# Optimization experiments

Hardware: AMD Instinct MI355X
Metric: run time of the kernel (lower is better)

Reference implementation:

```python
import jax, jax.numpy as jnp
import numpy as np

X_CH, Y_CH = 3, 31
C = X_CH + Y_CH            # s_channels = m_channels = 34
A = C * (C - 1) // 2       # 561 Givens rotation angles
SMIN, SMAX = 0.001, 1000.0


def setup_inputs() -> dict:
    key = jax.random.key(0)
    k1, k2 = jax.random.split(key)
    x = jax.random.normal(k1, (4, X_CH, 64, 64), dtype=jnp.float32)
    W = jax.random.normal(k2, (C + C + A, X_CH), dtype=jnp.float32) * 0.1
    b = jnp.zeros((C + C + A,), dtype=jnp.float32)
    return {"x": x, "W": W, "b": b}


def _covariance(s, a):
    # s: (B, C, H, W) positive variances; a: (B, A, H, W) rotation angles.
    B, _, H, Wd = s.shape
    cs = jnp.moveaxis(jnp.cos(a), 1, 0)  # (A, B, H, W)
    ss = jnp.moveaxis(jnp.sin(a), 1, 0)  # (A, B, H, W)
    ii, jj = np.triu_indices(C, k=1)      # same (i, j) order as the torch double loop
    ii = jnp.asarray(ii, dtype=jnp.int32)
    jj = jnp.asarray(jj, dtype=jnp.int32)

    # R starts as identity; each Givens rotation rij only mixes columns i and j
    # of R (R <- R @ rij), so we update two columns instead of a full matmul.
    R0 = jnp.broadcast_to(jnp.eye(C, dtype=s.dtype), (B, H, Wd, C, C))

    def step(R, inp):
        c_, s_, i, j = inp
        col_i = R[..., i]                      # (B, H, W, C)
        col_j = R[..., j]
        c_ = c_[..., None]
        s_ = s_[..., None]
        R = R.at[..., i].set(c_ * col_i + s_ * col_j)
        R = R.at[..., j].set(-s_ * col_i + c_ * col_j)
        return R, None

    R, _ = jax.lax.scan(step, R0, (cs, ss, ii, jj))
    sp = jnp.transpose(s, (0, 2, 3, 1))        # (B, H, W, C)
    # S = R^T D R with D = diag(sp): S[k,n] = sum_m R[m,k] * sp[m] * R[m,n]
    S = jnp.einsum('bhwmk,bhwm,bhwmn->bhwkn', R, sp, R)
    D = jnp.zeros((B, H, Wd, C, C), dtype=s.dtype).at[..., jnp.arange(C), jnp.arange(C)].set(sp)
    return S, R, D


def reference(x, W, b):
    # 1x1-conv encoder: (B, 3, H, W) -> (B, 629, H, W)
    w = jnp.einsum('oc,bchw->bohw', W, x) + b[None, :, None, None]
    m = jnp.transpose(w[:, :C], (0, 2, 3, 1))                  # (B, H, W, C) mean
    s = jax.nn.sigmoid(w[:, C:2 * C])
    s = SMIN * (1.0 - s) + SMAX * s                            # (B, C, H, W)
    a = jnp.pi * jnp.tanh(w[:, 2 * C:])                        # (B, A, H, W)
    S, _, _ = _covariance(s, a)
    return m, S, s
```

## Files before the change

kernel.cpp:

```cpp
#include <hip/hip_runtime.h>


#define CCH 34
#define ACH 561
#define HWPIX 4096
#define NPIX 16384
#define PXB 14
#define NPR 7
#define NTHR 256
#define CSLEN 141
#define CSPAIR (CSLEN * 16)
#define VROW 36
#define VPX (17 * VROW * 4)
#define OFF_S 557056
#define OFF_s 19496960
#define LOG2E 1.4426950408889634f

typedef float    f32x2 __attribute__((ext_vector_type(2)));
typedef _Float16 h2    __attribute__((ext_vector_type(2)));

struct Pairs {
    short i[ACH]; short j[ACH];
    constexpr Pairs() : i(), j() {
        int p = 0;
        for (int a = 0; a < CCH - 1; ++a)
            for (int b = a + 1; b < CCH; ++b) { i[p] = (short)a; j[p] = (short)b; ++p; }
    }
};
__device__ constexpr Pairs PR{};

__device__ __forceinline__ float dot2h(h2 a, h2 b, float c) {
#if __has_builtin(__builtin_amdgcn_fdot2)
    return __builtin_amdgcn_fdot2(a, b, c, false);
#else
    return fmaf((float)a[0], (float)b[0], fmaf((float)a[1], (float)b[1], c));
#endif
}

__device__ __forceinline__ void rot2(f32x2& Ri, f32x2& Rj, f32x2 c2, f32x2 s2) {
    f32x2 t1, t2;
    asm("v_pk_mul_f32 %0, %1, %2" : "=v"(t1) : "v"(s2), "v"(Rj));
    asm("v_pk_mul_f32 %0, %1, %2" : "=v"(t2) : "v"(s2), "v"(Ri));
    asm("v_pk_fma_f32 %0, %1, %2, %3" : "=v"(Ri) : "v"(c2), "v"(Ri), "v"(t1));
    asm("v_pk_fma_f32 %0, %1, %2, %3 neg_lo:[0,0,1] neg_hi:[0,0,1]"
        : "=v"(Rj) : "v"(c2), "v"(Rj), "v"(t2));
}

template <int P0, int P1>
__device__ __forceinline__ void apply_rots(f32x2* R2, const float4* cs) {
    #pragma unroll
    for (int k = P0; k < P1; ++k) {
        float4 cc = cs[k - P0];
        f32x2 c2; c2[0] = cc.x; c2[1] = cc.y;
        f32x2 s2; s2[0] = cc.z; s2[1] = cc.w;
        rot2(R2[PR.i[k]], R2[PR.j[k]], c2, s2);
    }
}

__device__ __forceinline__ float2 cs_of(float wv) {
    float e  = __builtin_amdgcn_exp2f((2.0f * LOG2E) * wv);
    float tt = 1.0f - 2.0f * __builtin_amdgcn_rcpf(e + 1.0f);
    float rv = 0.5f * tt;
    return make_float2(__builtin_amdgcn_cosf(rv), __builtin_amdgcn_sinf(rv));
}

template <int G0, int LEN>
__device__ __forceinline__ void fill_cs(const float* __restrict__ Wm,
                                        const float* __restrict__ bvec,
                                        const float* xs, char* ldsbuf,
                                        int npr, int t) {
    for (int o = t; o < npr * LEN; o += NTHR) {
        int pr = (int)((unsigned)o / (unsigned)LEN);
        int l  = o - pr * LEN;
        int ch = 2 * CCH + G0 + l;
        float w0 = Wm[ch * 3 + 0], w1 = Wm[ch * 3 + 1], w2 = Wm[ch * 3 + 2];
        float bb = bvec[ch];
        int pa = 2 * pr, pb = 2 * pr + 1;
        float2 A = cs_of(fmaf(w0, xs[pa*3+0], fmaf(w1, xs[pa*3+1], w2 * xs[pa*3+2])) + bb);
        float2 B = cs_of(fmaf(w0, xs[pb*3+0], fmaf(w1, xs[pb*3+1], w2 * xs[pb*3+2])) + bb);
        float4 cell; cell.x = A.x; cell.y = B.x; cell.z = A.y; cell.w = B.y;
        *(float4*)(ldsbuf + pr * CSPAIR + l * 16) = cell;
    }
}

__global__ __launch_bounds__(NTHR, 5) void gpd_kernel(
    const float* __restrict__ x,
    const float* __restrict__ Wm,
    const float* __restrict__ bvec,
    float* __restrict__ out)
{
    __shared__ alignas(16) char ldsbuf[NPR * VPX];
    __shared__ _Float16 lds_sh[PXB * CCH];
    __shared__ float xs[PXB * 3];

    const int t   = threadIdx.x;
    const int p0  = blockIdx.x * PXB;
    const int npx = min(PXB, NPIX - p0);
    const int npr = (npx + 1) >> 1;

    for (int i = t; i < npx * 3; i += NTHR) {
        int px = (int)((unsigned)i / 3u); int c = i - px * 3;
        int p = p0 + px; int b = p >> 12; int hw = p & 4095;
        xs[i] = x[(b * 3 + c) * HWPIX + hw];
    }
    __syncthreads();

    for (int o = t; o < npx * 68; o += NTHR) {
        int q = (int)((unsigned)o / 68u); int ch = o - q * 68;
        int p = p0 + q; int b = p >> 12; int hw = p & 4095;
        float wv = fmaf(Wm[ch*3+0], xs[q*3+0],
                   fmaf(Wm[ch*3+1], xs[q*3+1], Wm[ch*3+2] * xs[q*3+2])) + bvec[ch];
        if (ch < CCH) {
            out[(size_t)p * CCH + ch] = wv;
        } else {
            float e  = __builtin_amdgcn_exp2f(-wv * LOG2E);
            float sg = __builtin_amdgcn_rcpf(1.0f + e);
            float sv = fmaf(999.999f, sg, 0.001f);
            int c = ch - CCH;
            out[OFF_s + (size_t)(b * CCH + c) * HWPIX + hw] = sv;
            lds_sh[q * CCH + c] = (_Float16)sv;
        }
    }

    const int pr = t / CCH;
    const int m  = t - pr * CCH;
    const bool act = (t < npr * CCH);

    f32x2 R2[CCH];
    #pragma unroll
    for (int k = 0; k < CCH; ++k) { R2[k][0] = (k == m) ? 1.0f : 0.0f; R2[k][1] = R2[k][0]; }

    fill_cs<0, 141>(Wm, bvec, xs, ldsbuf, npr, t);
    __syncthreads();
    if (act) apply_rots<0, 141>(R2, (const float4*)(ldsbuf + pr * CSPAIR));
    __syncthreads();
    fill_cs<141, 140>(Wm, bvec, xs, ldsbuf, npr, t);
    __syncthreads();
    if (act) apply_rots<141, 281>(R2, (const float4*)(ldsbuf + pr * CSPAIR));
    __syncthreads();
    fill_cs<281, 140>(Wm, bvec, xs, ldsbuf, npr, t);
    __syncthreads();
    if (act) apply_rots<281, 421>(R2, (const float4*)(ldsbuf + pr * CSPAIR));
    __syncthreads();
    fill_cs<421, 140>(Wm, bvec, xs, ldsbuf, npr, t);
    __syncthreads();
    if (act) apply_rots<421, 561>(R2, (const float4*)(ldsbuf + pr * CSPAIR));
    __syncthreads();

    h2 Rh[CCH];
    #pragma unroll
    for (int n = 0; n < CCH; ++n) {
#if __has_builtin(__builtin_amdgcn_cvt_pkrtz)
        Rh[n] = __builtin_bit_cast(h2, __builtin_amdgcn_cvt_pkrtz(R2[n][0], R2[n][1]));
#else
        h2 hv; hv[0] = (_Float16)R2[n][0]; hv[1] = (_Float16)R2[n][1]; Rh[n] = hv;
#endif
    }

    #pragma unroll
    for (int h = 0; h < 2; ++h) {
        if (act) {
            char* base = ldsbuf + pr * VPX + (m >> 1) * (VROW * 4) + (m & 1) * 2;
            #pragma unroll
            for (int n = 0; n < CCH; ++n)
                *(_Float16*)(base + n * 4) = Rh[n][h];
        }
        __syncthreads();

        if (act) {
            const int px = 2 * pr + h;
            const unsigned* vb = (const unsigned*)(ldsbuf + pr * VPX);
            const _Float16* sh = lds_sh + px * CCH;
            float acc[CCH];
            #pragma unroll
            for (int n = 0; n < CCH; ++n) acc[n] = 0.0f;
            for (int mp = 0; mp < 17; ++mp) {
                const unsigned* row = vb + mp * VROW;
                h2 vk = __builtin_bit_cast(h2, row[m]) * *(const h2*)(sh + 2 * mp);
                #pragma unroll
                for (int g = 0; g < 8; ++g) {
                    uint4 rr = *(const uint4*)(row + 4 * g);
                    acc[4*g+0] = dot2h(vk, __builtin_bit_cast(h2, rr.x), acc[4*g+0]);
                    acc[4*g+1] = dot2h(vk, __builtin_bit_cast(h2, rr.y), acc[4*g+1]);
                    acc[4*g+2] = dot2h(vk, __builtin_bit_cast(h2, rr.z), acc[4*g+2]);
                    acc[4*g+3] = dot2h(vk, __builtin_bit_cast(h2, rr.w), acc[4*g+3]);
                }
                uint2 rr2 = *(const uint2*)(row + 32);
                acc[32] = dot2h(vk, __builtin_bit_cast(h2, rr2.x), acc[32]);
                acc[33] = dot2h(vk, __builtin_bit_cast(h2, rr2.y), acc[33]);
            }
            float* os = out + OFF_S + (size_t)(p0 + px) * (CCH * CCH) + m * CCH;
            #pragma unroll
            for (int n2 = 0; n2 < 17; ++n2) {
                float2 v; v.x = acc[2*n2]; v.y = acc[2*n2+1];
                *(float2*)(os + 2 * n2) = v;
            }
        }
        __syncthreads();
    }
}

extern "C" void kernel_launch(void* const* d_in, const int* in_sizes, int n_in,
                              void* d_out, int out_size, void* d_ws, size_t ws_size,
                              hipStream_t stream) {
    const float* x  = (const float*)d_in[0];
    const float* W  = (const float*)d_in[1];
    const float* bv = (const float*)d_in[2];
    float* out = (float*)d_out;
    const int nblk = (NPIX + PXB - 1) / PXB;
    hipLaunchKernelGGL(gpd_kernel, dim3(nblk), dim3(NTHR), 0, stream,
                       x, W, bv, out);
}
```

Baseline: 74.79 us.

## Assign one pixel pair per wavefront and drop block-wide barriers

Restructures the kernel so each 64-lane wavefront owns one pixel pair, with a private LDS region for cos/sin tables, R matrices and variances. All __syncthreads calls go away, and the angle tables are filled in two chunks instead of four. The launch becomes NPIX/8 blocks, and launch bounds drop from 5 to 4. The cost is that only 34 of 64 lanes do the rotation and covariance work, versus about 238 of 256 before. The code also relies on lockstep wavefront execution for LDS visibility without explicit barriers.

```diff
diff --git a/kernel.cpp b/kernel.cpp
--- a/kernel.cpp
+++ b/kernel.cpp
@@ -5,13 +5,12 @@
 #define ACH 561
 #define HWPIX 4096
 #define NPIX 16384
-#define PXB 14
-#define NPR 7
 #define NTHR 256
-#define CSLEN 141
-#define CSPAIR (CSLEN * 16)
+#define CH0 281
 #define VROW 36
 #define VPX (17 * VROW * 4)
+#define SH_OFF (2 * VPX)
+#define WREGB 5056
 #define OFF_S 557056
 #define OFF_s 19496960
 #define LOG2E 1.4426950408889634f
@@ -67,85 +66,80 @@
 template <int G0, int LEN>
 __device__ __forceinline__ void fill_cs(const float* __restrict__ Wm,
                                         const float* __restrict__ bvec,
-                                        const float* xs, char* ldsbuf,
-                                        int npr, int t) {
-    for (int o = t; o < npr * LEN; o += NTHR) {
-        int pr = (int)((unsigned)o / (unsigned)LEN);
-        int l  = o - pr * LEN;
+                                        char* wreg, int lane,
+                                        float xA0, float xA1, float xA2,
+                                        float xB0, float xB1, float xB2) {
+    for (int l = lane; l < LEN; l += 64) {
         int ch = 2 * CCH + G0 + l;
         float w0 = Wm[ch * 3 + 0], w1 = Wm[ch * 3 + 1], w2 = Wm[ch * 3 + 2];
         float bb = bvec[ch];
-        int pa = 2 * pr, pb = 2 * pr + 1;
-        float2 A = cs_of(fmaf(w0, xs[pa*3+0], fmaf(w1, xs[pa*3+1], w2 * xs[pa*3+2])) + bb);
-        float2 B = cs_of(fmaf(w0, xs[pb*3+0], fmaf(w1, xs[pb*3+1], w2 * xs[pb*3+2])) + bb);
+        float2 A = cs_of(fmaf(w0, xA0, fmaf(w1, xA1, w2 * xA2)) + bb);
+        float2 B = cs_of(fmaf(w0, xB0, fmaf(w1, xB1, w2 * xB2)) + bb);
         float4 cell; cell.x = A.x; cell.y = B.x; cell.z = A.y; cell.w = B.y;
-        *(float4*)(ldsbuf + pr * CSPAIR + l * 16) = cell;
-    }
-}
-
-__global__ __launch_bounds__(NTHR, 5) void gpd_kernel(
+        *(float4*)(wreg + l * 16) = cell;
+    }
+}
+
+__global__ __launch_bounds__(NTHR, 4) void gpd_kernel(
     const float* __restrict__ x,
     const float* __restrict__ Wm,
     const float* __restrict__ bvec,
     float* __restrict__ out)
 {
-    __shared__ alignas(16) char ldsbuf[NPR * VPX];
-    __shared__ _Float16 lds_sh[PXB * CCH];
-    __shared__ float xs[PXB * 3];
-
-    const int t   = threadIdx.x;
-    const int p0  = blockIdx.x * PXB;
-    const int npx = min(PXB, NPIX - p0);
-    const int npr = (npx + 1) >> 1;
-
-    for (int i = t; i < npx * 3; i += NTHR) {
-        int px = (int)((unsigned)i / 3u); int c = i - px * 3;
-        int p = p0 + px; int b = p >> 12; int hw = p & 4095;
-        xs[i] = x[(b * 3 + c) * HWPIX + hw];
-    }
-    __syncthreads();
-
-    for (int o = t; o < npx * 68; o += NTHR) {
-        int q = (int)((unsigned)o / 68u); int ch = o - q * 68;
-        int p = p0 + q; int b = p >> 12; int hw = p & 4095;
-        float wv = fmaf(Wm[ch*3+0], xs[q*3+0],
-                   fmaf(Wm[ch*3+1], xs[q*3+1], Wm[ch*3+2] * xs[q*3+2])) + bvec[ch];
+    __shared__ alignas(16) char lds[4 * WREGB];
+
+    const int t    = threadIdx.x;
+    const int lane = t & 63;
+    const int wv   = t >> 6;
+    char* wreg = lds + wv * WREGB;
+
+    const int pairp = blockIdx.x * 4 + wv;
+    const int pxA = 2 * pairp, pxB = pxA + 1;
+    const int bA = pxA >> 12, hwA = pxA & 4095;
+    const int bB = pxB >> 12, hwB = pxB & 4095;
+
+    const float xA0 = x[(bA*3+0)*HWPIX + hwA];
+    const float xA1 = x[(bA*3+1)*HWPIX + hwA];
+    const float xA2 = x[(bA*3+2)*HWPIX + hwA];
+    const float xB0 = x[(bB*3+0)*HWPIX + hwB];
+    const float xB1 = x[(bB*3+1)*HWPIX + hwB];
+    const float xB2 = x[(bB*3+2)*HWPIX + hwB];
+
+    _Float16* sh = (_Float16*)(wreg + SH_OFF);
+
+    for (int o = lane; o < 2 * 68; o += 64) {
+        int half = o >= 68;
+        int ch   = o - 68 * half;
+        float x0 = half ? xB0 : xA0;
+        float x1 = half ? xB1 : xA1;
+        float x2 = half ? xB2 : xA2;
+        int px = pxA + half;
+        int b = px >> 12, hw = px & 4095;
+        float wvv = fmaf(Wm[ch*3+0], x0,
+                    fmaf(Wm[ch*3+1], x1, Wm[ch*3+2] * x2)) + bvec[ch];
         if (ch < CCH) {
-            out[(size_t)p * CCH + ch] = wv;
+            out[(size_t)px * CCH + ch] = wvv;
         } else {
-            float e  = __builtin_amdgcn_exp2f(-wv * LOG2E);
+            float e  = __builtin_amdgcn_exp2f(-wvv * LOG2E);
             float sg = __builtin_amdgcn_rcpf(1.0f + e);
             float sv = fmaf(999.999f, sg, 0.001f);
             int c = ch - CCH;
             out[OFF_s + (size_t)(b * CCH + c) * HWPIX + hw] = sv;
-            lds_sh[q * CCH + c] = (_Float16)sv;
+            sh[half * CCH + c] = (_Float16)sv;
         }
     }
 
-    const int pr = t / CCH;
-    const int m  = t - pr * CCH;
-    const bool act = (t < npr * CCH);
+    const int m = lane;
+    const bool act = (lane < CCH);
 
     f32x2 R2[CCH];
     #pragma unroll
     for (int k = 0; k < CCH; ++k) { R2[k][0] = (k == m) ? 1.0f : 0.0f; R2[k][1] = R2[k][0]; }
 
-    fill_cs<0, 141>(Wm, bvec, xs, ldsbuf, npr, t);
-    __syncthreads();
-    if (act) apply_rots<0, 141>(R2, (const float4*)(ldsbuf + pr * CSPAIR));
-    __syncthreads();
-    fill_cs<141, 140>(Wm, bvec, xs, ldsbuf, npr, t);
-    __syncthreads();
-    if (act) apply_rots<141, 281>(R2, (const float4*)(ldsbuf + pr * CSPAIR));
-    __syncthreads();
-    fill_cs<281, 140>(Wm, bvec, xs, ldsbuf, npr, t);
-    __syncthreads();
-    if (act) apply_rots<281, 421>(R2, (const float4*)(ldsbuf + pr * CSPAIR));
-    __syncthreads();
-    fill_cs<421, 140>(Wm, bvec, xs, ldsbuf, npr, t);
-    __syncthreads();
-    if (act) apply_rots<421, 561>(R2, (const float4*)(ldsbuf + pr * CSPAIR));
-    __syncthreads();
+    fill_cs<0, CH0>(Wm, bvec, wreg, lane, xA0, xA1, xA2, xB0, xB1, xB2);
+    if (act) apply_rots<0, CH0>(R2, (const float4*)wreg);
+    fill_cs<CH0, ACH - CH0>(Wm, bvec, wreg, lane, xA0, xA1, xA2, xB0, xB1, xB2);
+    if (act) apply_rots<CH0, ACH>(R2, (const float4*)wreg);
 
     h2 Rh[CCH];
     #pragma unroll
@@ -157,26 +151,26 @@
 #endif
     }
 
+    if (act) {
+        char* baseA = wreg + (m >> 1) * (VROW * 4) + (m & 1) * 2;
+        #pragma unroll
+        for (int n = 0; n < CCH; ++n) {
+            *(_Float16*)(baseA + n * 4)       = Rh[n][0];
+            *(_Float16*)(baseA + VPX + n * 4) = Rh[n][1];
+        }
+    }
+
     #pragma unroll
     for (int h = 0; h < 2; ++h) {
         if (act) {
-            char* base = ldsbuf + pr * VPX + (m >> 1) * (VROW * 4) + (m & 1) * 2;
-            #pragma unroll
-            for (int n = 0; n < CCH; ++n)
-                *(_Float16*)(base + n * 4) = Rh[n][h];
-        }
-        __syncthreads();
-
-        if (act) {
-            const int px = 2 * pr + h;
-            const unsigned* vb = (const unsigned*)(ldsbuf + pr * VPX);
-            const _Float16* sh = lds_sh + px * CCH;
+            const unsigned* vb = (const unsigned*)(wreg + h * VPX);
+            const _Float16* shp = sh + h * CCH;
             float acc[CCH];
             #pragma unroll
             for (int n = 0; n < CCH; ++n) acc[n] = 0.0f;
             for (int mp = 0; mp < 17; ++mp) {
                 const unsigned* row = vb + mp * VROW;
-                h2 vk = __builtin_bit_cast(h2, row[m]) * *(const h2*)(sh + 2 * mp);
+                h2 vk = __builtin_bit_cast(h2, row[m]) * *(const h2*)(shp + 2 * mp);
                 #pragma unroll
                 for (int g = 0; g < 8; ++g) {
                     uint4 rr = *(const uint4*)(row + 4 * g);
@@ -189,14 +183,13 @@
                 acc[32] = dot2h(vk, __builtin_bit_cast(h2, rr2.x), acc[32]);
                 acc[33] = dot2h(vk, __builtin_bit_cast(h2, rr2.y), acc[33]);
             }
-            float* os = out + OFF_S + (size_t)(p0 + px) * (CCH * CCH) + m * CCH;
+            float* os = out + OFF_S + (size_t)(pxA + h) * (CCH * CCH) + m * CCH;
             #pragma unroll
             for (int n2 = 0; n2 < 17; ++n2) {
                 float2 v; v.x = acc[2*n2]; v.y = acc[2*n2+1];
                 *(float2*)(os + 2 * n2) = v;
             }
         }
-        __syncthreads();
     }
 }
 
@@ -207,7 +200,6 @@
     const float* W  = (const float*)d_in[1];
     const float* bv = (const float*)d_in[2];
     float* out = (float*)d_out;
-    const int nblk = (NPIX + PXB - 1) / PXB;
-    hipLaunchKernelGGL(gpd_kernel, dim3(nblk), dim3(NTHR), 0, stream,
+    hipLaunchKernelGGL(gpd_kernel, dim3(NPIX / 8), dim3(NTHR), 0, stream,
                        x, W, bv, out);
 }
```

New measurement: 89.88 us. 20.2% more time.
